# Performance work log

Hardware: AMD Instinct MI355X
Metric: run time of the kernel (lower is better)

Reference implementation:

```python
import jax, jax.numpy as jnp
import numpy as np

D_MODEL = 1024
N_HEADS = 16
D_HEAD = 64
TOTAL = N_HEADS * D_HEAD


def setup_inputs() -> dict:
    key = jax.random.key(0)
    k1, k2, k3 = jax.random.split(key, 3)
    x = jax.random.normal(k1, (2, 2048, D_MODEL), dtype=jnp.float32)
    W_qkv = jax.random.normal(k2, (3 * TOTAL, D_MODEL), dtype=jnp.float32) * 0.02
    W_out = jax.random.normal(k3, (D_MODEL, TOTAL), dtype=jnp.float32) * 0.02
    return {"x": x, "W_qkv": W_qkv, "W_out": W_out}


def reference(x, W_qkv, W_out):
    B, T, D = x.shape
    scale = D_HEAD ** -0.5
    qkv = jnp.einsum('btd,ed->bte', x, W_qkv)  # [B,T,3*TOTAL]
    q, k, v = jnp.split(qkv, 3, axis=-1)
    def heads(t):
        return t.reshape(B, T, N_HEADS, D_HEAD).transpose(0, 2, 1, 3)  # [B,H,T,Dh]
    q, k, v = heads(q), heads(k), heads(v)
    scores = jnp.einsum('bhqd,bhkd->bhqk', q, k) * scale
    causal = jnp.tril(jnp.ones((T, T), dtype=bool))
    scores = jnp.where(causal[None, None], scores, -jnp.inf)
    attn = jax.nn.softmax(scores, axis=-1)
    out = jnp.einsum('bhqk,bhkd->bhqd', attn, v)
    out = out.transpose(0, 2, 1, 3).reshape(B, T, TOTAL)
    return jnp.einsum('bte,de->btd', out, W_out)
```

## Files before the change

kernel.cpp:

```cpp
#include <hip/hip_runtime.h>
#include <hip/hip_bf16.h>

typedef __attribute__((ext_vector_type(4))) float f32x4;
typedef __attribute__((ext_vector_type(8))) short s16x8;
typedef __attribute__((ext_vector_type(4))) short s16x4;

#define DEV static __device__ __forceinline__

DEV unsigned short f2bf(float f) {
    unsigned int u = __builtin_bit_cast(unsigned int, f);
    u += 0x7fffu + ((u >> 16) & 1u);
    return (unsigned short)(u >> 16);
}

#if __has_builtin(__builtin_amdgcn_exp2f)
#define EXP2(x) __builtin_amdgcn_exp2f(x)
#else
#define EXP2(x) exp2f(x)
#endif

DEV unsigned int pack2(float a, float b) {
#if __has_builtin(__builtin_amdgcn_perm)
    return __builtin_amdgcn_perm(__builtin_bit_cast(unsigned int, b),
                                 __builtin_bit_cast(unsigned int, a), 0x07060302u);
#else
    return (__builtin_bit_cast(unsigned int, a) >> 16) |
           (__builtin_bit_cast(unsigned int, b) & 0xffff0000u);
#endif
}

DEV s16x8 ld8(const unsigned short* p) {
    s16x4 lo = *(const s16x4*)(p);
    s16x4 hi = *(const s16x4*)(p + 4);
    return __builtin_shufflevector(lo, hi, 0, 1, 2, 3, 4, 5, 6, 7);
}
DEV s16x8 ld8a(const unsigned short* p) { return *(const s16x8*)p; }

DEV f32x4 mfma16(s16x8 a, s16x8 b, f32x4 c) {
    return __builtin_amdgcn_mfma_f32_16x16x32_bf16(a, b, c, 0, 0, 0);
}

DEV void glds16(const unsigned short* g, unsigned short* l) {
    __builtin_amdgcn_global_load_lds(
        (const __attribute__((address_space(1))) unsigned int*)g,
        (__attribute__((address_space(3))) unsigned int*)l, 16, 0, 0);
}

__global__ __launch_bounds__(256) void convf2b2(
        const float* __restrict__ s0, unsigned short* __restrict__ d0, int n40,
        const float* __restrict__ s1, unsigned short* __restrict__ d1, int n41) {
    int i = blockIdx.x * 256 + threadIdx.x;
    if (i < n40) {
        float4 v = ((const float4*)s0)[i];
        s16x4 o = {(short)f2bf(v.x), (short)f2bf(v.y), (short)f2bf(v.z), (short)f2bf(v.w)};
        ((s16x4*)d0)[i] = o;
    } else if (i - n40 < n41) {
        int j = i - n40;
        float4 v = ((const float4*)s1)[j];
        s16x4 o = {(short)f2bf(v.x), (short)f2bf(v.y), (short)f2bf(v.z), (short)f2bf(v.w)};
        ((s16x4*)d1)[j] = o;
    }
}

__global__ __launch_bounds__(256) void convf2b(const float* __restrict__ s,
                                               unsigned short* __restrict__ d, int n4) {
    int i = blockIdx.x * 256 + threadIdx.x;
    if (i < n4) {
        float4 v = ((const float4*)s)[i];
        s16x4 o = {(short)f2bf(v.x), (short)f2bf(v.y), (short)f2bf(v.z), (short)f2bf(v.w)};
        ((s16x4*)d)[i] = o;
    }
}

__global__ __launch_bounds__(512) void qkv_gemm(
        const unsigned short* __restrict__ Xb, const unsigned short* __restrict__ Wq,
        unsigned short* __restrict__ q_ws, unsigned short* __restrict__ k_ws,
        unsigned short* __restrict__ v_ws) {
    __shared__ unsigned short As[2][128 * 32];
    __shared__ unsigned short Bs[2][128 * 32];
    const int tid = threadIdx.x, lane = tid & 63, wave = tid >> 6;
    const int l15 = lane & 15, l4 = lane >> 4;
    const int wm = (wave >> 1) * 32, wn = (wave & 1) * 64;
    const int m0 = blockIdx.y * 128, n0 = blockIdx.x * 128;

    f32x4 acc[2][4];
    for (int i = 0; i < 2; i++)
        for (int j = 0; j < 4; j++) acc[i][j] = (f32x4){0.f, 0.f, 0.f, 0.f};

    const unsigned short* aptr = &Xb[(size_t)(m0 + wave * 16 + (lane >> 2)) * 1024 + (lane & 3) * 8];
    const unsigned short* bptr = &Wq[(size_t)(n0 + wave * 16 + (lane >> 2)) * 1024 + (lane & 3) * 8];

    for (int k0 = 0; k0 < 1024; k0 += 64) {
        __syncthreads();
        for (int c = 0; c < 2; c++) {
            glds16(aptr + k0 + c * 32, &As[c][(wave * 16) * 32]);
            glds16(bptr + k0 + c * 32, &Bs[c][(wave * 16) * 32]);
        }
        __syncthreads();
        for (int c = 0; c < 2; c++) {
            s16x8 af[2], bf[4];
            for (int mt = 0; mt < 2; mt++) af[mt] = ld8a(&As[c][(wm + mt * 16 + l15) * 32 + l4 * 8]);
            for (int nt = 0; nt < 4; nt++) bf[nt] = ld8a(&Bs[c][(wn + nt * 16 + l15) * 32 + l4 * 8]);
            for (int mt = 0; mt < 2; mt++)
                for (int nt = 0; nt < 4; nt++)
                    acc[mt][nt] = mfma16(af[mt], bf[nt], acc[mt][nt]);
        }
    }

    const int gnb = n0 + wn;
    const int which = gnb >> 10, h = (gnb >> 6) & 15;
    const int bidx = m0 >> 11, tb = m0 & 2047;
    if (which == 2) {
        unsigned short* dst = v_ws + (size_t)(bidx * 16 + h) * 64 * 2048;
        for (int mt = 0; mt < 2; mt++) {
            int t = tb + wm + mt * 16 + l4 * 4;
            for (int nt = 0; nt < 4; nt++) {
                int dh = nt * 16 + l15;
                s16x4 pp;
                for (int r = 0; r < 4; r++) pp[r] = (short)f2bf(acc[mt][nt][r]);
                *(s16x4*)&dst[(size_t)dh * 2048 + t] = pp;
            }
        }
    } else {
        unsigned short* dst = ((which == 0) ? q_ws : k_ws) + (size_t)(bidx * 16 + h) * 2048 * 64;
        const float sc = (which == 0) ? 0.18033688f : 1.0f;
        for (int mt = 0; mt < 2; mt++) {
            int t0 = tb + wm + mt * 16 + l4 * 4;
            for (int nt = 0; nt < 4; nt++) {
                int dh = nt * 16 + l15;
                for (int r = 0; r < 4; r++)
                    dst[(size_t)(t0 + r) * 64 + dh] = f2bf(acc[mt][nt][r] * sc);
            }
        }
    }
}

__global__ __launch_bounds__(512) void attn(
        const unsigned short* __restrict__ q_ws, const unsigned short* __restrict__ k_ws,
        const unsigned short* __restrict__ v_ws, unsigned short* __restrict__ ao) {
    constexpr int LDP = 68;
    __shared__ unsigned short Ks[2][2][64 * 32];
    __shared__ unsigned short Vt[2][2][64 * 32];
    __shared__ unsigned short Ps[8 * 16 * LDP];
    const int tid = threadIdx.x, lane = tid & 63, wave = tid >> 6;
    const int l15 = lane & 15, l4 = lane >> 4;
    const int bh = blockIdx.x, b = bh >> 4, h = bh & 15;
    const int q0 = (15 - blockIdx.y) * 128;
    const int qw0 = q0 + wave * 16;
    const size_t base = (size_t)bh * 2048 * 64;
    const unsigned short* vtb = v_ws + (size_t)bh * 64 * 2048;
    unsigned short* Pw = &Ps[wave * 16 * LDP];

    const int seg = wave & 3, half = wave >> 2;
    const unsigned short* kg0 = &k_ws[base + (size_t)(seg * 16 + (lane >> 2)) * 64 + half * 32 + (lane & 3) * 8];
    const unsigned short* vg0 = &vtb[(size_t)(seg * 16 + (lane >> 2)) * 2048 + half * 32 + (lane & 3) * 8];
    unsigned short* kl[2] = {&Ks[0][half][(seg * 16) * 32], &Ks[1][half][(seg * 16) * 32]};
    unsigned short* vl[2] = {&Vt[0][half][(seg * 16) * 32], &Vt[1][half][(seg * 16) * 32]};

    s16x8 qf[2];
    for (int c = 0; c < 2; c++)
        qf[c] = ld8a(&q_ws[base + (size_t)(qw0 + l15) * 64 + c * 32 + l4 * 8]);

    f32x4 o[4];
    for (int i = 0; i < 4; i++) o[i] = (f32x4){0.f, 0.f, 0.f, 0.f};
    float lsum = 0.f;

    glds16(kg0, kl[0]);
    glds16(vg0, vl[0]);

    const int kend = q0 + 128;
    for (int k0 = 0; k0 < kend; k0 += 64) {
        const int cur = (k0 >> 6) & 1;
        __syncthreads();
        if (k0 + 64 < kend) {
            glds16(kg0 + (size_t)(k0 + 64) * 64, kl[cur ^ 1]);
            glds16(vg0 + (k0 + 64), vl[cur ^ 1]);
        }

        if (k0 < qw0 + 16) {
            f32x4 st[4];
            for (int ks = 0; ks < 4; ks++) st[ks] = (f32x4){0.f, 0.f, 0.f, 0.f};
            for (int c = 0; c < 2; c++)
                for (int ks = 0; ks < 4; ks++) {
                    s16x8 kf = ld8a(&Ks[cur][c][(ks * 16 + l15) * 32 + l4 * 8]);
                    st[ks] = mfma16(kf, qf[c], st[ks]);
                }

            if (k0 + 63 > qw0) {
                int qg = qw0 + l15;
                for (int ks = 0; ks < 4; ks++)
                    for (int r = 0; r < 4; r++) {
                        int kg = k0 + ks * 16 + l4 * 4 + r;
                        if (kg > qg) st[ks][r] = -1e30f;
                    }
            }
            float part = 0.f;
            for (int ks = 0; ks < 4; ks++) {
                float p0 = EXP2(st[ks][0]);
                float p1 = EXP2(st[ks][1]);
                float p2 = EXP2(st[ks][2]);
                float p3 = EXP2(st[ks][3]);
                part += (p0 + p1) + (p2 + p3);
                unsigned int u0 = pack2(p0, p1), u1 = pack2(p2, p3);
                *(uint2*)&Pw[l15 * LDP + ks * 16 + l4 * 4] = (uint2){u0, u1};
            }
            lsum += part;

            s16x8 pf[2];
            for (int c = 0; c < 2; c++)
                pf[c] = ld8(&Pw[l15 * LDP + c * 32 + l4 * 8]);
            for (int c = 0; c < 2; c++)
                for (int ds = 0; ds < 4; ds++) {
                    s16x8 vf = ld8a(&Vt[cur][c][(ds * 16 + l15) * 32 + l4 * 8]);
                    o[ds] = mfma16(vf, pf[c], o[ds]);
                }
        }
    }

    float t = lsum;
    t += __shfl_xor(t, 16, 64);
    t += __shfl_xor(t, 32, 64);
    float inv = 1.f / t;
    for (int ds = 0; ds < 4; ds++) {
        s16x4 pp;
        for (int r = 0; r < 4; r++) pp[r] = (short)f2bf(o[ds][r] * inv);
        *(s16x4*)&Pw[l15 * LDP + ds * 16 + l4 * 4] = pp;
    }
    int qr = lane >> 2, qt = lane & 3;
    size_t orow = ((size_t)b * 2048 + q0 + wave * 16 + qr) * 1024 + h * 64 + qt * 16;
    *(s16x8*)&ao[orow]     = ld8(&Pw[qr * LDP + qt * 16]);
    *(s16x8*)&ao[orow + 8] = ld8(&Pw[qr * LDP + qt * 16 + 8]);
}

__global__ __launch_bounds__(256) void out_gemm(
        const unsigned short* __restrict__ A, const unsigned short* __restrict__ Bm,
        float* __restrict__ OUT) {
    __shared__ unsigned short As[2][128 * 32];
    __shared__ unsigned short Bs[2][64 * 32];
    const int tid = threadIdx.x, lane = tid & 63, wave = tid >> 6;
    const int l15 = lane & 15, l4 = lane >> 4;
    const int wm = wave * 32;
    const int m0 = blockIdx.y * 128, n0 = blockIdx.x * 64;

    f32x4 acc[2][4];
    for (int i = 0; i < 2; i++)
        for (int j = 0; j < 4; j++) acc[i][j] = (f32x4){0.f, 0.f, 0.f, 0.f};

    const unsigned short* aptr = &A[(size_t)(m0 + wave * 32 + (lane >> 2)) * 1024 + (lane & 3) * 8];
    const unsigned short* bptr = &Bm[(size_t)(n0 + wave * 16 + (lane >> 2)) * 1024 + (lane & 3) * 8];

    for (int k0 = 0; k0 < 1024; k0 += 64) {
        __syncthreads();
        for (int c = 0; c < 2; c++) {
            glds16(aptr + k0 + c * 32, &As[c][(wave * 32) * 32]);
            glds16(aptr + k0 + c * 32 + 16 * 1024, &As[c][(wave * 32 + 16) * 32]);
            glds16(bptr + k0 + c * 32, &Bs[c][(wave * 16) * 32]);
        }
        __syncthreads();
        for (int c = 0; c < 2; c++) {
            s16x8 af[2], bf[4];
            for (int mt = 0; mt < 2; mt++) af[mt] = ld8a(&As[c][(wm + mt * 16 + l15) * 32 + l4 * 8]);
            for (int nt = 0; nt < 4; nt++) bf[nt] = ld8a(&Bs[c][(nt * 16 + l15) * 32 + l4 * 8]);
            for (int mt = 0; mt < 2; mt++)
                for (int nt = 0; nt < 4; nt++)
                    acc[mt][nt] = mfma16(af[mt], bf[nt], acc[mt][nt]);
        }
    }

    for (int mt = 0; mt < 2; mt++)
        for (int nt = 0; nt < 4; nt++)
            for (int r = 0; r < 4; r++) {
                int gm = m0 + wm + mt * 16 + l4 * 4 + r;
                int gn = n0 + nt * 16 + l15;
                OUT[(size_t)gm * 1024 + gn] = acc[mt][nt][r];
            }
}

extern "C" void kernel_launch(void* const* d_in, const int* in_sizes, int n_in,
                              void* d_out, int out_size, void* d_ws, size_t ws_size,
                              hipStream_t stream) {
    (void)in_sizes; (void)n_in; (void)out_size; (void)ws_size;
    const float* x    = (const float*)d_in[0];
    const float* Wqkv = (const float*)d_in[1];
    const float* Wout = (const float*)d_in[2];
    float* out = (float*)d_out;

    unsigned short* q_ws = (unsigned short*)d_ws;
    unsigned short* k_ws = q_ws + (size_t)4 * 1024 * 1024;
    unsigned short* v_ws = k_ws + (size_t)4 * 1024 * 1024;
    unsigned short* xb   = v_ws + (size_t)4 * 1024 * 1024;
    unsigned short* ao   = xb;
    unsigned short* wqb  = (unsigned short*)d_out;
    unsigned short* wob  = q_ws;

    const int n4x = 2 * 2048 * 1024 / 4, n4w = 3072 * 1024 / 4;
    convf2b2<<<(n4x + n4w + 255) / 256, 256, 0, stream>>>(x, xb, n4x, Wqkv, wqb, n4w);
    qkv_gemm<<<dim3(24, 32), 512, 0, stream>>>(xb, wqb, q_ws, k_ws, v_ws);
    attn<<<dim3(32, 16), 512, 0, stream>>>(q_ws, k_ws, v_ws, ao);
    convf2b<<<1024, 256, 0, stream>>>(Wout, wob, 1024 * 1024 / 4);
    out_gemm<<<dim3(16, 32), 256, 0, stream>>>(ao, wob, out);
}
```

Baseline: 173.5 us.

## Give each attention wave two query sub-tiles to reuse K/V fragments

The attention kernel drops from 8 waves of 16 query rows to 4 waves of 32 rows. Each K and V fragment read from LDS now feeds two MFMAs, which halves LDS fragment traffic per unit of compute. Each wave now issues both halves of the K/V tile loads itself. The query-tile order is also changed to interleave long and short causal tiles. In exchange, register pressure roughly doubles, there are fewer waves per block to hide latency, and causal masking is coarser, so some fully masked 16-row subtiles still get computed.

```diff
diff --git a/kernel.cpp b/kernel.cpp
--- a/kernel.cpp
+++ b/kernel.cpp
@@ -135,101 +135,129 @@
     }
 }
 
-__global__ __launch_bounds__(512) void attn(
+__global__ __launch_bounds__(256) void attn(
         const unsigned short* __restrict__ q_ws, const unsigned short* __restrict__ k_ws,
         const unsigned short* __restrict__ v_ws, unsigned short* __restrict__ ao) {
     constexpr int LDP = 68;
     __shared__ unsigned short Ks[2][2][64 * 32];
     __shared__ unsigned short Vt[2][2][64 * 32];
-    __shared__ unsigned short Ps[8 * 16 * LDP];
+    __shared__ unsigned short Ps[4 * 32 * LDP];
     const int tid = threadIdx.x, lane = tid & 63, wave = tid >> 6;
     const int l15 = lane & 15, l4 = lane >> 4;
     const int bh = blockIdx.x, b = bh >> 4, h = bh & 15;
-    const int q0 = (15 - blockIdx.y) * 128;
-    const int qw0 = q0 + wave * 16;
+    const int yy = blockIdx.y;
+    const int qtile = (yy < 8) ? (15 - yy) : (yy - 8);
+    const int q0 = qtile * 128;
+    const int qw0 = q0 + wave * 32;
     const size_t base = (size_t)bh * 2048 * 64;
     const unsigned short* vtb = v_ws + (size_t)bh * 64 * 2048;
-    unsigned short* Pw = &Ps[wave * 16 * LDP];
-
-    const int seg = wave & 3, half = wave >> 2;
-    const unsigned short* kg0 = &k_ws[base + (size_t)(seg * 16 + (lane >> 2)) * 64 + half * 32 + (lane & 3) * 8];
-    const unsigned short* vg0 = &vtb[(size_t)(seg * 16 + (lane >> 2)) * 2048 + half * 32 + (lane & 3) * 8];
-    unsigned short* kl[2] = {&Ks[0][half][(seg * 16) * 32], &Ks[1][half][(seg * 16) * 32]};
-    unsigned short* vl[2] = {&Vt[0][half][(seg * 16) * 32], &Vt[1][half][(seg * 16) * 32]};
-
-    s16x8 qf[2];
-    for (int c = 0; c < 2; c++)
-        qf[c] = ld8a(&q_ws[base + (size_t)(qw0 + l15) * 64 + c * 32 + l4 * 8]);
-
-    f32x4 o[4];
-    for (int i = 0; i < 4; i++) o[i] = (f32x4){0.f, 0.f, 0.f, 0.f};
-    float lsum = 0.f;
-
-    glds16(kg0, kl[0]);
-    glds16(vg0, vl[0]);
+    unsigned short* Pw = &Ps[wave * 32 * LDP];
+
+    const int seg = wave;
+    const unsigned short* kg0[2];
+    const unsigned short* vg0[2];
+    unsigned short* kl[2][2];
+    unsigned short* vl[2][2];
+    for (int hf = 0; hf < 2; hf++) {
+        kg0[hf] = &k_ws[base + (size_t)(seg * 16 + (lane >> 2)) * 64 + hf * 32 + (lane & 3) * 8];
+        vg0[hf] = &vtb[(size_t)(seg * 16 + (lane >> 2)) * 2048 + hf * 32 + (lane & 3) * 8];
+        for (int bu = 0; bu < 2; bu++) {
+            kl[bu][hf] = &Ks[bu][hf][(seg * 16) * 32];
+            vl[bu][hf] = &Vt[bu][hf][(seg * 16) * 32];
+        }
+    }
+
+    s16x8 qf[2][2];
+    for (int qs = 0; qs < 2; qs++)
+        for (int c = 0; c < 2; c++)
+            qf[qs][c] = ld8a(&q_ws[base + (size_t)(qw0 + qs * 16 + l15) * 64 + c * 32 + l4 * 8]);
+
+    f32x4 o[2][4];
+    for (int qs = 0; qs < 2; qs++)
+        for (int i = 0; i < 4; i++) o[qs][i] = (f32x4){0.f, 0.f, 0.f, 0.f};
+    float lsum[2] = {0.f, 0.f};
+
+    for (int hf = 0; hf < 2; hf++) {
+        glds16(kg0[hf], kl[0][hf]);
+        glds16(vg0[hf], vl[0][hf]);
+    }
 
     const int kend = q0 + 128;
     for (int k0 = 0; k0 < kend; k0 += 64) {
         const int cur = (k0 >> 6) & 1;
         __syncthreads();
         if (k0 + 64 < kend) {
-            glds16(kg0 + (size_t)(k0 + 64) * 64, kl[cur ^ 1]);
-            glds16(vg0 + (k0 + 64), vl[cur ^ 1]);
-        }
-
-        if (k0 < qw0 + 16) {
-            f32x4 st[4];
-            for (int ks = 0; ks < 4; ks++) st[ks] = (f32x4){0.f, 0.f, 0.f, 0.f};
+            for (int hf = 0; hf < 2; hf++) {
+                glds16(kg0[hf] + (size_t)(k0 + 64) * 64, kl[cur ^ 1][hf]);
+                glds16(vg0[hf] + (k0 + 64), vl[cur ^ 1][hf]);
+            }
+        }
+
+        if (k0 < qw0 + 32) {
+            f32x4 st[2][4];
+            for (int qs = 0; qs < 2; qs++)
+                for (int ks = 0; ks < 4; ks++) st[qs][ks] = (f32x4){0.f, 0.f, 0.f, 0.f};
             for (int c = 0; c < 2; c++)
                 for (int ks = 0; ks < 4; ks++) {
                     s16x8 kf = ld8a(&Ks[cur][c][(ks * 16 + l15) * 32 + l4 * 8]);
-                    st[ks] = mfma16(kf, qf[c], st[ks]);
+                    st[0][ks] = mfma16(kf, qf[0][c], st[0][ks]);
+                    st[1][ks] = mfma16(kf, qf[1][c], st[1][ks]);
                 }
 
             if (k0 + 63 > qw0) {
-                int qg = qw0 + l15;
-                for (int ks = 0; ks < 4; ks++)
-                    for (int r = 0; r < 4; r++) {
-                        int kg = k0 + ks * 16 + l4 * 4 + r;
-                        if (kg > qg) st[ks][r] = -1e30f;
-                    }
-            }
-            float part = 0.f;
-            for (int ks = 0; ks < 4; ks++) {
-                float p0 = EXP2(st[ks][0]);
-                float p1 = EXP2(st[ks][1]);
-                float p2 = EXP2(st[ks][2]);
-                float p3 = EXP2(st[ks][3]);
-                part += (p0 + p1) + (p2 + p3);
-                unsigned int u0 = pack2(p0, p1), u1 = pack2(p2, p3);
-                *(uint2*)&Pw[l15 * LDP + ks * 16 + l4 * 4] = (uint2){u0, u1};
-            }
-            lsum += part;
-
-            s16x8 pf[2];
-            for (int c = 0; c < 2; c++)
-                pf[c] = ld8(&Pw[l15 * LDP + c * 32 + l4 * 8]);
+                for (int qs = 0; qs < 2; qs++) {
+                    int qg = qw0 + qs * 16 + l15;
+                    for (int ks = 0; ks < 4; ks++)
+                        for (int r = 0; r < 4; r++) {
+                            int kg = k0 + ks * 16 + l4 * 4 + r;
+                            if (kg > qg) st[qs][ks][r] = -1e30f;
+                        }
+                }
+            }
+            for (int qs = 0; qs < 2; qs++) {
+                float part = 0.f;
+                for (int ks = 0; ks < 4; ks++) {
+                    float p0 = EXP2(st[qs][ks][0]);
+                    float p1 = EXP2(st[qs][ks][1]);
+                    float p2 = EXP2(st[qs][ks][2]);
+                    float p3 = EXP2(st[qs][ks][3]);
+                    part += (p0 + p1) + (p2 + p3);
+                    unsigned int u0 = pack2(p0, p1), u1 = pack2(p2, p3);
+                    *(uint2*)&Pw[(qs * 16 + l15) * LDP + ks * 16 + l4 * 4] = (uint2){u0, u1};
+                }
+                lsum[qs] += part;
+            }
+
+            s16x8 pf[2][2];
+            for (int qs = 0; qs < 2; qs++)
+                for (int c = 0; c < 2; c++)
+                    pf[qs][c] = ld8(&Pw[(qs * 16 + l15) * LDP + c * 32 + l4 * 8]);
             for (int c = 0; c < 2; c++)
                 for (int ds = 0; ds < 4; ds++) {
                     s16x8 vf = ld8a(&Vt[cur][c][(ds * 16 + l15) * 32 + l4 * 8]);
-                    o[ds] = mfma16(vf, pf[c], o[ds]);
+                    o[0][ds] = mfma16(vf, pf[0][c], o[0][ds]);
+                    o[1][ds] = mfma16(vf, pf[1][c], o[1][ds]);
                 }
         }
     }
 
-    float t = lsum;
-    t += __shfl_xor(t, 16, 64);
-    t += __shfl_xor(t, 32, 64);
-    float inv = 1.f / t;
-    for (int ds = 0; ds < 4; ds++) {
-        s16x4 pp;
-        for (int r = 0; r < 4; r++) pp[r] = (short)f2bf(o[ds][r] * inv);
-        *(s16x4*)&Pw[l15 * LDP + ds * 16 + l4 * 4] = pp;
-    }
-    int qr = lane >> 2, qt = lane & 3;
-    size_t orow = ((size_t)b * 2048 + q0 + wave * 16 + qr) * 1024 + h * 64 + qt * 16;
-    *(s16x8*)&ao[orow]     = ld8(&Pw[qr * LDP + qt * 16]);
-    *(s16x8*)&ao[orow + 8] = ld8(&Pw[qr * LDP + qt * 16 + 8]);
+    for (int qs = 0; qs < 2; qs++) {
+        float t = lsum[qs];
+        t += __shfl_xor(t, 16, 64);
+        t += __shfl_xor(t, 32, 64);
+        float inv = 1.f / t;
+        for (int ds = 0; ds < 4; ds++) {
+            s16x4 pp;
+            for (int r = 0; r < 4; r++) pp[r] = (short)f2bf(o[qs][ds][r] * inv);
+            *(s16x4*)&Pw[(qs * 16 + l15) * LDP + ds * 16 + l4 * 4] = pp;
+        }
+    }
+    for (int qs = 0; qs < 2; qs++) {
+        int qr = lane >> 2, qc = lane & 3;
+        size_t orow = ((size_t)b * 2048 + q0 + wave * 32 + qs * 16 + qr) * 1024 + h * 64 + qc * 16;
+        *(s16x8*)&ao[orow]     = ld8(&Pw[(qs * 16 + qr) * LDP + qc * 16]);
+        *(s16x8*)&ao[orow + 8] = ld8(&Pw[(qs * 16 + qr) * LDP + qc * 16 + 8]);
+    }
 }
 
 __global__ __launch_bounds__(256) void out_gemm(
@@ -296,7 +324,7 @@
     const int n4x = 2 * 2048 * 1024 / 4, n4w = 3072 * 1024 / 4;
     convf2b2<<<(n4x + n4w + 255) / 256, 256, 0, stream>>>(x, xb, n4x, Wqkv, wqb, n4w);
     qkv_gemm<<<dim3(24, 32), 512, 0, stream>>>(xb, wqb, q_ws, k_ws, v_ws);
-    attn<<<dim3(32, 16), 512, 0, stream>>>(q_ws, k_ws, v_ws, ao);
+    attn<<<dim3(32, 16), 256, 0, stream>>>(q_ws, k_ws, v_ws, ao);
     convf2b<<<1024, 256, 0, stream>>>(Wout, wob, 1024 * 1024 / 4);
     out_gemm<<<dim3(16, 32), 256, 0, stream>>>(ao, wob, out);
 }
```

After: 177.5 us. 2.3% more time.

## Balance causal attention blocks, triple-buffer K/V loads with swizzled LDS

Applied to the files above, without the earlier changes.

Each attention block now pairs a late and an early 64-row query tile, so every block does a similar amount of causal work, and the launch becomes a 1-D grid ordered to group heads. K/V staging moves from double to triple buffering, prefetching two tiles ahead with explicit vmcnt waits in place of a full __syncthreads. The LDS layout gets an XOR swizzle to reduce bank conflicts, and s_setprio is raised around the MFMA sections. LDS use grows and a min-blocks launch bound is added, which may limit registers.

```diff
diff --git a/kernel.cpp b/kernel.cpp
--- a/kernel.cpp
+++ b/kernel.cpp
@@ -135,63 +135,83 @@
     }
 }
 
-__global__ __launch_bounds__(512) void attn(
+__global__ __launch_bounds__(512, 4) void attn(
         const unsigned short* __restrict__ q_ws, const unsigned short* __restrict__ k_ws,
         const unsigned short* __restrict__ v_ws, unsigned short* __restrict__ ao) {
     constexpr int LDP = 68;
-    __shared__ unsigned short Ks[2][2][64 * 32];
-    __shared__ unsigned short Vt[2][2][64 * 32];
+    __shared__ unsigned short Ks[3][2][64 * 32];
+    __shared__ unsigned short Vt[3][2][64 * 32];
     __shared__ unsigned short Ps[8 * 16 * LDP];
     const int tid = threadIdx.x, lane = tid & 63, wave = tid >> 6;
     const int l15 = lane & 15, l4 = lane >> 4;
-    const int bh = blockIdx.x, b = bh >> 4, h = bh & 15;
-    const int q0 = (15 - blockIdx.y) * 128;
-    const int qw0 = q0 + wave * 16;
+    const int xf = (l15 >> 1) & 3;
+
+    const int id = blockIdx.x;
+    const int bh8 = id & 7, rest = id >> 3;
+    const int qq = rest & 15, g = rest >> 4;
+    const int bh = bh8 + 8 * g, b = bh >> 4, h = bh & 15;
+    const int p = (g < 2) ? qq : 15 - qq;
+    const int qrow = ((wave < 4) ? (31 - p) : p) * 64 + (wave & 3) * 16;
+    const int nt = 32 - p;
+
     const size_t base = (size_t)bh * 2048 * 64;
     const unsigned short* vtb = v_ws + (size_t)bh * 64 * 2048;
     unsigned short* Pw = &Ps[wave * 16 * LDP];
 
-    const int seg = wave & 3, half = wave >> 2;
-    const unsigned short* kg0 = &k_ws[base + (size_t)(seg * 16 + (lane >> 2)) * 64 + half * 32 + (lane & 3) * 8];
-    const unsigned short* vg0 = &vtb[(size_t)(seg * 16 + (lane >> 2)) * 2048 + half * 32 + (lane & 3) * 8];
-    unsigned short* kl[2] = {&Ks[0][half][(seg * 16) * 32], &Ks[1][half][(seg * 16) * 32]};
-    unsigned short* vl[2] = {&Vt[0][half][(seg * 16) * 32], &Vt[1][half][(seg * 16) * 32]};
+    const int seg = wave >> 1, hf = wave & 1;
+    const int srow = lane >> 2;
+    const int scol = ((lane & 3) ^ ((lane >> 3) & 3)) * 8;
+    const unsigned short* kg = &k_ws[base + (size_t)(seg * 16 + srow) * 64 + hf * 32 + scol];
+    const unsigned short* vg = &vtb[(size_t)(seg * 16 + srow) * 2048 + hf * 32 + scol];
+    unsigned short* kld = &Ks[0][hf][(seg * 16) * 32];
+    unsigned short* vld = &Vt[0][hf][(seg * 16) * 32];
+    const unsigned short* krd = &Ks[0][0][0];
+    const unsigned short* vrd = &Vt[0][0][0];
 
     s16x8 qf[2];
     for (int c = 0; c < 2; c++)
-        qf[c] = ld8a(&q_ws[base + (size_t)(qw0 + l15) * 64 + c * 32 + l4 * 8]);
+        qf[c] = ld8a(&q_ws[base + (size_t)(qrow + l15) * 64 + c * 32 + l4 * 8]);
+    asm volatile("s_waitcnt vmcnt(0)" ::: "memory");
 
     f32x4 o[4];
     for (int i = 0; i < 4; i++) o[i] = (f32x4){0.f, 0.f, 0.f, 0.f};
     float lsum = 0.f;
 
-    glds16(kg0, kl[0]);
-    glds16(vg0, vl[0]);
-
-    const int kend = q0 + 128;
-    for (int k0 = 0; k0 < kend; k0 += 64) {
-        const int cur = (k0 >> 6) & 1;
-        __syncthreads();
-        if (k0 + 64 < kend) {
-            glds16(kg0 + (size_t)(k0 + 64) * 64, kl[cur ^ 1]);
-            glds16(vg0 + (k0 + 64), vl[cur ^ 1]);
-        }
-
-        if (k0 < qw0 + 16) {
+    glds16(kg, kld);
+    glds16(vg, vld);
+    glds16(kg + 4096, kld + 4096);
+    glds16(vg + 64, vld + 4096);
+
+    int cur = 0;
+    for (int r = 0; r < nt; ++r) {
+        if (r + 1 < nt) asm volatile("s_waitcnt vmcnt(2)" ::: "memory");
+        else            asm volatile("s_waitcnt vmcnt(0)" ::: "memory");
+        __builtin_amdgcn_s_barrier();
+        if (r + 2 < nt) {
+            const int nb = (cur == 0) ? 2 : cur - 1;
+            glds16(kg + (size_t)(r + 2) * 4096, kld + nb * 4096);
+            glds16(vg + (r + 2) * 64,           vld + nb * 4096);
+        }
+        const int k0 = r * 64;
+        if (k0 < qrow + 16) {
+            const unsigned short* kb = krd + cur * 4096;
+            const unsigned short* vb = vrd + cur * 4096;
             f32x4 st[4];
             for (int ks = 0; ks < 4; ks++) st[ks] = (f32x4){0.f, 0.f, 0.f, 0.f};
+            __builtin_amdgcn_s_setprio(1);
             for (int c = 0; c < 2; c++)
                 for (int ks = 0; ks < 4; ks++) {
-                    s16x8 kf = ld8a(&Ks[cur][c][(ks * 16 + l15) * 32 + l4 * 8]);
+                    s16x8 kf = ld8a(&kb[c * 2048 + (ks * 16 + l15) * 32 + (l4 ^ xf) * 8]);
                     st[ks] = mfma16(kf, qf[c], st[ks]);
                 }
-
-            if (k0 + 63 > qw0) {
-                int qg = qw0 + l15;
+            __builtin_amdgcn_s_setprio(0);
+
+            if (k0 + 63 > qrow) {
+                int qg = qrow + l15;
                 for (int ks = 0; ks < 4; ks++)
-                    for (int r = 0; r < 4; r++) {
-                        int kg = k0 + ks * 16 + l4 * 4 + r;
-                        if (kg > qg) st[ks][r] = -1e30f;
+                    for (int rr = 0; rr < 4; rr++) {
+                        int kgi = k0 + ks * 16 + l4 * 4 + rr;
+                        if (kgi > qg) st[ks][rr] = -1e30f;
                     }
             }
             float part = 0.f;
@@ -209,12 +229,15 @@
             s16x8 pf[2];
             for (int c = 0; c < 2; c++)
                 pf[c] = ld8(&Pw[l15 * LDP + c * 32 + l4 * 8]);
+            __builtin_amdgcn_s_setprio(1);
             for (int c = 0; c < 2; c++)
                 for (int ds = 0; ds < 4; ds++) {
-                    s16x8 vf = ld8a(&Vt[cur][c][(ds * 16 + l15) * 32 + l4 * 8]);
+                    s16x8 vf = ld8a(&vb[c * 2048 + (ds * 16 + l15) * 32 + (l4 ^ xf) * 8]);
                     o[ds] = mfma16(vf, pf[c], o[ds]);
                 }
-        }
+            __builtin_amdgcn_s_setprio(0);
+        }
+        cur = (cur == 2) ? 0 : cur + 1;
     }
 
     float t = lsum;
@@ -227,7 +250,7 @@
         *(s16x4*)&Pw[l15 * LDP + ds * 16 + l4 * 4] = pp;
     }
     int qr = lane >> 2, qt = lane & 3;
-    size_t orow = ((size_t)b * 2048 + q0 + wave * 16 + qr) * 1024 + h * 64 + qt * 16;
+    size_t orow = ((size_t)b * 2048 + qrow + qr) * 1024 + h * 64 + qt * 16;
     *(s16x8*)&ao[orow]     = ld8(&Pw[qr * LDP + qt * 16]);
     *(s16x8*)&ao[orow + 8] = ld8(&Pw[qr * LDP + qt * 16 + 8]);
 }
@@ -296,7 +319,7 @@
     const int n4x = 2 * 2048 * 1024 / 4, n4w = 3072 * 1024 / 4;
     convf2b2<<<(n4x + n4w + 255) / 256, 256, 0, stream>>>(x, xb, n4x, Wqkv, wqb, n4w);
     qkv_gemm<<<dim3(24, 32), 512, 0, stream>>>(xb, wqb, q_ws, k_ws, v_ws);
-    attn<<<dim3(32, 16), 512, 0, stream>>>(q_ws, k_ws, v_ws, ao);
+    attn<<<dim3(512), 512, 0, stream>>>(q_ws, k_ws, v_ws, ao);
     convf2b<<<1024, 256, 0, stream>>>(Wout, wob, 1024 * 1024 / 4);
     out_gemm<<<dim3(16, 32), 256, 0, stream>>>(ao, wob, out);
 }
```

Measured after the change: 165.0 us. 4.9% less time.
